# Performance work log

Hardware: AMD Instinct MI355X
Metric: run time of the kernel (lower is better)

The kernel has to match this reference:

```python
import jax, jax.numpy as jnp
import numpy as np

B, N_PER, E_PER = 100, 1000, 12000  # graphs, nodes/graph, edges/graph
N, E = B * N_PER, B * E_PER
K = int(np.ceil(0.8 * N_PER))  # TopKPooling ratio=0.8 -> 800 kept nodes/graph


def setup_inputs() -> dict:
    key = jax.random.key(0)
    ks = jax.random.split(key, 16)
    g = jnp.repeat(jnp.arange(B, dtype=jnp.int64), E_PER)
    src = g * N_PER + jax.random.randint(ks[0], (E,), 0, N_PER)
    dst = g * N_PER + jax.random.randint(ks[1], (E,), 0, N_PER)
    edge_index = jnp.stack([src, dst]).astype(jnp.int64)
    edge_attr = jax.random.uniform(ks[2], (E,), dtype=jnp.float32) + 0.1  # positive edge weights
    x = jax.random.normal(ks[3], (N, 3), dtype=jnp.float32)
    batch = jnp.repeat(jnp.arange(B, dtype=jnp.int64), N_PER)
    s = 0.1
    return {
        'x': x, 'edge_index': edge_index, 'edge_attr': edge_attr, 'batch': batch,
        'conv1_w': jax.random.normal(ks[4], (3, 64), dtype=jnp.float32) * s,
        'conv1_b': jnp.zeros((64,), dtype=jnp.float32),
        'conv2_w': jax.random.normal(ks[5], (64, 64), dtype=jnp.float32) * s,
        'conv2_b': jnp.zeros((64,), dtype=jnp.float32),
        'pool_w': jax.random.normal(ks[6], (64,), dtype=jnp.float32) * s,
        'lin1_w': jax.random.normal(ks[7], (64, 64), dtype=jnp.float32) * s,
        'lin1_b': jnp.zeros((64,), dtype=jnp.float32),
        'lin2_w': jax.random.normal(ks[8], (64, 32), dtype=jnp.float32) * s,
        'lin2_b': jnp.zeros((32,), dtype=jnp.float32),
        'lin3_w': jax.random.normal(ks[9], (32, 1), dtype=jnp.float32) * s,
        'lin3_b': jnp.zeros((1,), dtype=jnp.float32),
    }


def gcn_conv(x, row, col, ew, W, b):
    # PyG GCNConv with edge_weight and implicit self-loops (weight 1):
    # deg[i] = sum_{e: col=i} ew[e] + 1;  norm_e = d^{-1/2}[row]*ew*d^{-1/2}[col]
    h = x @ W  # [N, out]
    deg = jax.ops.segment_sum(ew, col, num_segments=N) + 1.0
    dinv = jax.lax.rsqrt(deg)
    msg = (dinv[row] * ew * dinv[col])[:, None] * h[row]  # [E, out]
    out = jax.ops.segment_sum(msg, col, num_segments=N)
    out = out + (dinv * dinv)[:, None] * h  # self-loop term
    return out + b


def reference(x, edge_index, edge_attr, batch, conv1_w, conv1_b, conv2_w, conv2_b,
              pool_w, lin1_w, lin1_b, lin2_w, lin2_b, lin3_w, lin3_b):
    row, col = edge_index[0], edge_index[1]
    h = jax.nn.relu(gcn_conv(x, row, col, edge_attr, conv1_w, conv1_b))
    x1 = h.reshape(B, N_PER, 64).mean(axis=1)  # global_mean_pool (equal-size graphs)
    h = jax.nn.relu(gcn_conv(h, row, col, edge_attr, conv2_w, conv2_b))
    # TopKPooling: score = tanh(x.w / ||w||), keep top-K per graph, gate by score
    score = jnp.tanh(h @ pool_w / jnp.linalg.norm(pool_w))  # [N]
    score_bn = score.reshape(B, N_PER)
    vals, idx = jax.lax.top_k(score_bn, K)  # [B, K]
    h_bn = h.reshape(B, N_PER, 64)
    h_sel = jnp.take_along_axis(h_bn, idx[..., None], axis=1) * vals[..., None]
    x2 = h_sel.mean(axis=1)  # global_mean_pool on pooled graph
    z = x1 + x2
    z = jax.nn.relu(z @ lin1_w + lin1_b)
    z = jax.nn.relu(z @ lin2_w + lin2_b)  # dropout is identity in eval mode
    out = jax.nn.sigmoid(z @ lin3_w + lin3_b)[:, 0]
    return out
```

## Files before the change

### kernel.cpp

```cpp
#include <hip/hip_runtime.h>

#define B_G   100
#define N_PER 1000
#define E_PER 12000
#define NTOT  (B_G * N_PER)
#define ETOT  (B_G * E_PER)
#define KSEL  800
#define EPT   12

#define CSRB  0u
#define ENDB  4915200u
#define H2B   5324800u
#define KEYB  11878400u
#define X1BB  12697600u
#define WSNEED 12723200u

typedef __attribute__((ext_vector_type(8))) short short8;
typedef __attribute__((ext_vector_type(4))) float float4_;

__device__ __forceinline__ unsigned short f2bf(float f) {
    unsigned u = __float_as_uint(f);
    u += 0x7fffu + ((u >> 16) & 1u);
    return (unsigned short)(u >> 16);
}
__device__ __forceinline__ float upk(unsigned q) {
    return __uint_as_float(q & 0xFFFF0000u);
}
__device__ __forceinline__ float dec_raw(unsigned byte7f) {
    return __uint_as_float(byte7f << 20);
}
__device__ __forceinline__ unsigned enc_fp8(float z) {
    unsigned u = __float_as_uint(z * 0x1p-120f);
    u += 0x7FFFFu + ((u >> 20) & 1u);
    return u >> 20;
}

#define BUILD_BODY(PRE) do {                                                   \
    int esrc[EPT], edst[EPT]; float eww[EPT];                                  \
    int ne = (tid < (E_PER - (EPT - 1) * 1024)) ? EPT : EPT - 1;               \
    _Pragma("unroll")                                                          \
    for (int i = 0; i < EPT; i++) {                                            \
        if (i < ne) {                                                          \
            int e = tid + i * 1024;                                            \
            esrc[i] = ei[ebase + e] - gbase;                                   \
            edst[i] = ei[ETOT + ebase + e] - gbase;                            \
            eww[i]  = ew[ebase + e];                                           \
        }                                                                      \
    }                                                                          \
    ends[tid] = 0;                                                             \
    PRE                                                                        \
    __syncthreads();                                                           \
    _Pragma("unroll")                                                          \
    for (int i = 0; i < EPT; i++)                                              \
        if (i < ne) atomicAdd(&ends[edst[i]], 1);                              \
    __syncthreads();                                                           \
    int v = ends[tid];                                                         \
    int sc = v;                                                                \
    _Pragma("unroll")                                                          \
    for (int m = 1; m < 64; m <<= 1) {                                         \
        int t = __shfl_up(sc, m);                                              \
        if (lane >= m) sc += t;                                                \
    }                                                                          \
    if (lane == 63) wpart[wid] = sc;                                           \
    __syncthreads();                                                           \
    if (tid < 16) {                                                            \
        int s2 = wpart[tid];                                                   \
        _Pragma("unroll")                                                      \
        for (int m = 1; m < 16; m <<= 1) {                                     \
            int t = __shfl_up(s2, m);                                          \
            if (tid >= m) s2 += t;                                             \
        }                                                                      \
        wpart[tid] = s2;                                                       \
    }                                                                          \
    __syncthreads();                                                           \
    int incl = sc + (wid > 0 ? wpart[wid - 1] : 0);                            \
    ends[tid] = incl;                                                          \
    posc[tid] = incl - v;                                                      \
    __syncthreads();                                                           \
    _Pragma("unroll")                                                          \
    for (int i = 0; i < EPT; i++)                                              \
        if (i < ne) {                                                          \
            int p = atomicAdd(&posc[edst[i]], 1);                              \
            csr[p] = ((unsigned)f2bf(eww[i]) << 16) | (unsigned)esrc[i];       \
        }                                                                      \
    __syncthreads();                                                           \
} while (0)

#define REST_BODY() do {                                                       \
    float dmy = 0.f;                                                           \
    int s0i = 0, e0i = 0;                                                      \
    if (tid < N_PER) {                                                         \
        s0i = tid ? ends[tid - 1] : 0;                                         \
        e0i = ends[tid];                                                       \
        float s0 = 0.f, s1 = 0.f;                                              \
        int k = s0i;                                                           \
        for (; k + 2 <= e0i; k += 2) { s0 += upk(csr[k]); s1 += upk(csr[k + 1]); } \
        if (k < e0i) s0 += upk(csr[k]);                                        \
        dmy = rsqrtf(s0 + s1 + 1.0f);                                          \
        dl[tid] = dmy;                                                         \
        xl[tid * 3 + 0] *= dmy;                                                \
        xl[tid * 3 + 1] *= dmy;                                                \
        xl[tid * 3 + 2] *= dmy;                                                \
    }                                                                          \
    __syncthreads();                                                           \
    if (tid < N_PER) {                                                         \
        float a0 = xl[tid * 3 + 0], a1 = xl[tid * 3 + 1], a2 = xl[tid * 3 + 2];\
        for (int k = s0i; k < e0i; k++) {                                      \
            unsigned q = csr[k];                                               \
            int i0 = (int)(q & 0xFFFFu) * 3;                                   \
            float wv = upk(q);                                                 \
            a0 += wv * xl[i0]; a1 += wv * xl[i0 + 1]; a2 += wv * xl[i0 + 2];   \
        }                                                                      \
        aggv[tid * 3 + 0] = dmy * a0;                                          \
        aggv[tid * 3 + 1] = dmy * a1;                                          \
        aggv[tid * 3 + 2] = dmy * a2;                                          \
    }                                                                          \
    __syncthreads();                                                           \
    {                                                                          \
        float w0 = w1[lane], w1v = w1[64 + lane], w2v = w1[128 + lane], bf = b1[lane]; \
        float* sred = (float*)(uA + 12288);                                    \
        float px = 0.f;                                                        \
        int chunk = (lane & 31) >> 3;                                          \
        int word  = ((lane >= 32) ? 2 : 0) + ((lane & 7) >> 2);                \
        for (int node = wid; node < N_PER; node += 16) {                       \
            float a0 = aggv[node * 3], a1 = aggv[node * 3 + 1], a2 = aggv[node * 3 + 2]; \
            float hv = fmaxf(a0 * w0 + a1 * w1v + a2 * w2v + bf, 0.f);         \
            px += hv;                                                          \
            unsigned byte = enc_fp8(dl[node] * hv);                            \
            unsigned t1 = __shfl_xor(byte, 1);                                 \
            unsigned v16 = (lane & 1) ? (t1 | (byte << 8)) : (byte | (t1 << 8)); \
            unsigned t2 = __shfl_xor(v16, 2);                                  \
            unsigned v32 = (lane & 2) ? (t2 | (v16 << 16)) : (v16 | (t2 << 16)); \
            if ((lane & 3) == 0) {                                             \
                int cs = chunk ^ ((node >> 1) & 3);                            \
                *(unsigned*)(zs + node * 64 + cs * 16 + word * 4) = v32;       \
            }                                                                  \
        }                                                                      \
        sred[wid * 64 + lane] = px;                                            \
        __syncthreads();                                                       \
        if (tid < 64) {                                                        \
            float t = 0.f;                                                     \
            for (int r = 0; r < 16; r++) t += sred[r * 64 + tid];              \
            x1b[tid] = t * (1.0f / N_PER);                                     \
        }                                                                      \
    }                                                                          \
} while (0)

#define CONV2_TI(TI, AF0, AF1) do {                                            \
    const int t_ = wid + (TI) * 16;                                            \
    const int li_ = t_ * 16 + nloc;                                            \
    const bool valid_ = li_ < N_PER;                                           \
    float acc_[16];                                                            \
    int s_ = 0, cn_ = 0;                                                       \
    if (valid_) {                                                              \
        uint4 rv_ = *(const uint4*)(zs + li_ * 64 + ((kgrp ^ ((li_ >> 1) & 3)) << 4)); \
        _Pragma("unroll")                                                      \
        for (int j = 0; j < 4; j++) {                                          \
            acc_[j]      = dec_raw((rv_.x >> (8 * j)) & 0x7Fu);                \
            acc_[4 + j]  = dec_raw((rv_.y >> (8 * j)) & 0x7Fu);                \
            acc_[8 + j]  = dec_raw((rv_.z >> (8 * j)) & 0x7Fu);                \
            acc_[12 + j] = dec_raw((rv_.w >> (8 * j)) & 0x7Fu);                \
        }                                                                      \
        s_ = li_ ? ends[li_ - 1] : 0;                                          \
        cn_ = ends[li_] - s_;                                                  \
    } else {                                                                   \
        _Pragma("unroll")                                                      \
        for (int j = 0; j < 16; j++) acc_[j] = 0.f;                            \
    }                                                                          \
    int mx_ = cn_;                                                             \
    _Pragma("unroll")                                                          \
    for (int m = 1; m < 16; m <<= 1) mx_ = max(mx_, __shfl_xor(mx_, m));       \
    for (int k = 0; k < mx_; k++) {                                            \
        if (k < cn_) {                                                         \
            unsigned q_ = csr[s_ + k];                                         \
            int src_ = (int)(q_ & 0xFFFFu);                                    \
            float wv_ = upk(q_);                                               \
            uint4 rv_ = *(const uint4*)(zs + src_ * 64 + ((kgrp ^ ((src_ >> 1) & 3)) << 4)); \
            _Pragma("unroll")                                                  \
            for (int j = 0; j < 4; j++) {                                      \
                acc_[j]      += wv_ * dec_raw((rv_.x >> (8 * j)) & 0x7Fu);     \
                acc_[4 + j]  += wv_ * dec_raw((rv_.y >> (8 * j)) & 0x7Fu);     \
                acc_[8 + j]  += wv_ * dec_raw((rv_.z >> (8 * j)) & 0x7Fu);     \
                acc_[12 + j] += wv_ * dec_raw((rv_.w >> (8 * j)) & 0x7Fu);     \
            }                                                                  \
        }                                                                      \
    }                                                                          \
    float scale_ = (valid_ ? dl[li_] : 0.f) * 0x1p120f;                        \
    _Pragma("unroll")                                                          \
    for (int j = 0; j < 8; j++) {                                              \
        AF0[j] = (short)f2bf(scale_ * acc_[j]);                                \
        AF1[j] = (short)f2bf(scale_ * acc_[8 + j]);                            \
    }                                                                          \
} while (0)

#define W2_TI(TI, AF0, AF1) do {                                               \
    const int t_ = wid + (TI) * 16;                                            \
    if (t_ < 63) {                                                             \
        float4_ accv_[4];                                                      \
        _Pragma("unroll")                                                      \
        for (int c = 0; c < 4; ++c) accv_[c] = (float4_){0.f, 0.f, 0.f, 0.f};  \
        _Pragma("unroll")                                                      \
        for (int c = 0; c < 4; ++c) {                                          \
            accv_[c] = __builtin_amdgcn_mfma_f32_16x16x32_bf16(AF0, Bf[0][c], accv_[c], 0, 0, 0); \
            accv_[c] = __builtin_amdgcn_mfma_f32_16x16x32_bf16(AF1, Bf[1][c], accv_[c], 0, 0, 0); \
        }                                                                      \
        _Pragma("unroll")                                                      \
        for (int r2 = 0; r2 < 4; ++r2) {                                       \
            int li2_ = t_ * 16 + kgrp * 4 + r2;                                \
            bool valid2_ = li2_ < N_PER;                                       \
            float sp_ = 0.f;                                                   \
            _Pragma("unroll")                                                  \
            for (int c = 0; c < 4; ++c) {                                      \
                float hv_ = fmaxf(accv_[c][r2] + b2c[c], 0.f);                 \
                sp_ += hv_ * pwc[c];                                           \
                if (valid2_) zs[li2_ * 64 + c * 16 + nloc] = (unsigned char)enc_fp8(hv_); \
            }                                                                  \
            _Pragma("unroll")                                                  \
            for (int m = 1; m < 16; m <<= 1) sp_ += __shfl_xor(sp_, m);        \
            if (valid2_ && nloc == 0) {                                        \
                float scv_ = tanhf(sp_ * invn);                                \
                unsigned bits_ = __float_as_uint(scv_);                        \
                unsigned u_ = (bits_ & 0x80000000u) ? ~bits_ : (bits_ | 0x80000000u); \
                keys[li2_] = ((unsigned long long)u_ << 32) | (unsigned)(1023 - li2_); \
            }                                                                  \
        }                                                                      \
    }                                                                          \
} while (0)

#define W2_SETUP() do {                                                        \
    _Pragma("unroll")                                                          \
    for (int kh = 0; kh < 2; ++kh)                                             \
        _Pragma("unroll")                                                      \
        for (int c = 0; c < 4; ++c) {                                          \
            short8 t;                                                          \
            _Pragma("unroll")                                                  \
            for (int j = 0; j < 8; ++j)                                        \
                t[j] = (short)f2bf(w2[(kh * 32 + kgrp * 8 + j) * 64 + c * 16 + nloc]); \
            Bf[kh][c] = t;                                                     \
        }                                                                      \
    _Pragma("unroll")                                                          \
    for (int c = 0; c < 4; ++c) {                                              \
        b2c[c] = b2[c * 16 + nloc];                                            \
        pwc[c] = pw[c * 16 + nloc];                                            \
    }                                                                          \
    {                                                                          \
        float p = pw[lane], pn = p * p;                                        \
        _Pragma("unroll")                                                      \
        for (int m = 32; m; m >>= 1) pn += __shfl_xor(pn, m);                  \
        invn = rsqrtf(pn);                                                     \
    }                                                                          \
} while (0)

#define TAIL_BODY(OUTIDX) do {                                                 \
    {                                                                          \
        unsigned long long key = keys[tid];                                    \
        for (int k = 2; k <= 1024; k <<= 1) {                                  \
            for (int j = k >> 1; j > 0; j >>= 1) {                             \
                bool desc = (tid & k) == 0;                                    \
                unsigned long long p;                                          \
                if (j >= 64) {                                                 \
                    keys[tid] = key;                                           \
                    __syncthreads();                                           \
                    p = keys[tid ^ j];                                         \
                    __syncthreads();                                           \
                } else {                                                       \
                    p = __shfl_xor(key, j);                                    \
                }                                                              \
                bool low = (tid & j) == 0;                                     \
                bool sw = low ? (desc ? (key < p) : (key > p))                 \
                              : (desc ? (p < key) : (p > key));                \
                if (sw) key = p;                                               \
            }                                                                  \
        }                                                                      \
        keys[tid] = key;                                                       \
    }                                                                          \
    __syncthreads();                                                           \
    {                                                                          \
        int f = tid & 63, w16 = tid >> 6;                                      \
        float acc2 = 0.f;                                                      \
        for (int r = w16; r < KSEL; r += 16) {                                 \
            unsigned long long key = keys[r];                                  \
            int idx = 1023 - (int)(key & 0xFFFFFFFFu);                         \
            unsigned u = (unsigned)(key >> 32);                                \
            unsigned bits = (u & 0x80000000u) ? (u & 0x7FFFFFFFu) : ~u;        \
            float valS = __uint_as_float(bits) * 0x1p120f;                     \
            acc2 += valS * dec_raw((unsigned)zs[idx * 64 + f] & 0x7Fu);        \
        }                                                                      \
        red[tid] = acc2;                                                       \
    }                                                                          \
    __syncthreads();                                                           \
    if (tid < 64) {                                                            \
        float s2 = 0.f;                                                        \
        for (int ww = 0; ww < 16; ww++) s2 += red[ww * 64 + tid];              \
        zbuf[tid] = x1b[tid] + s2 * (1.0f / KSEL);                             \
    }                                                                          \
    __syncthreads();                                                           \
    if (tid < 64) {                                                            \
        float a = l1b[tid];                                                    \
        for (int k = 0; k < 64; k++) a += zbuf[k] * l1w[k * 64 + tid];         \
        a1buf[tid] = fmaxf(a, 0.f);                                            \
    }                                                                          \
    __syncthreads();                                                           \
    if (tid < 32) {                                                            \
        float a = l2b[tid];                                                    \
        for (int k = 0; k < 64; k++) a += a1buf[k] * l2w[k * 32 + tid];        \
        a2buf[tid] = fmaxf(a, 0.f);                                            \
    }                                                                          \
    __syncthreads();                                                           \
    if (tid == 0) {                                                            \
        float t = l3b[0];                                                      \
        for (int k = 0; k < 32; k++) t += a2buf[k] * l3w[k];                   \
        out[OUTIDX] = 1.0f / (1.0f + expf(-t));                                \
    }                                                                          \
} while (0)

#define SMEM_DECLS()                                                           \
    __shared__ __align__(16) unsigned char smem[136832];                       \
    unsigned char* zs = smem;                                                  \
    float* xl = (float*)smem;                                                  \
    unsigned* csr = (unsigned*)(smem + 64000);                                 \
    int*   ends = (int*)(smem + 112000);                                       \
    float* dl   = (float*)(smem + 116096);                                     \
    int*   posc = (int*)(smem + 116096);                                       \
    int*   wpart = (int*)(smem + 120192);                                      \
    float* x1b   = (float*)(smem + 120192);                                    \
    unsigned char* uA = smem + 120448;                                         \
    float* aggv = (float*)uA;                                                  \
    (void)posc; (void)wpart; (void)aggv;

__global__ __launch_bounds__(1024) void k_build(
    const int* __restrict__ ei, const float* __restrict__ ew,
    unsigned char* __restrict__ ws) {
    __shared__ __align__(16) unsigned csr[12000];
    __shared__ int ends[1024];
    __shared__ int posc[1024];
    __shared__ int wpart[16];
    int g = blockIdx.x, tid = threadIdx.x;
    int wid = tid >> 6, lane = tid & 63;
    int gbase = g * N_PER, ebase = g * E_PER;
    BUILD_BODY();
    {
        uint4* cw = (uint4*)(ws + CSRB + (size_t)g * 49152);
        const uint4* cs = (const uint4*)csr;
        for (int i = tid; i < 3000; i += 1024) cw[i] = cs[i];
        ((int*)(ws + ENDB + (size_t)g * 4096))[tid] = ends[tid];
    }
}

__global__ __launch_bounds__(1024)
__attribute__((amdgpu_waves_per_eu(4, 4))) void k_mid(
    const float* __restrict__ x,
    const float* __restrict__ w1, const float* __restrict__ b1,
    const float* __restrict__ w2, const float* __restrict__ b2,
    const float* __restrict__ pw, unsigned char* __restrict__ ws) {
    SMEM_DECLS();
    int g = blockIdx.x >> 1, half = blockIdx.x & 1, tid = threadIdx.x;
    int wid = tid >> 6, lane = tid & 63;
    int gbase = g * N_PER;
    {
        const uint4* cs = (const uint4*)(ws + CSRB + (size_t)g * 49152);
        uint4* cd = (uint4*)csr;
        for (int i = tid; i < 3000; i += 1024) cd[i] = cs[i];
        ends[tid] = ((const int*)(ws + ENDB + (size_t)g * 4096))[tid];
        for (int i = tid; i < N_PER * 3; i += 1024) xl[i] = x[(size_t)gbase * 3 + i];
    }
    __syncthreads();
    REST_BODY();
    int kgrp = lane >> 4, nloc = lane & 15;
    const int tiA = half * 2, tiB = half * 2 + 1;
    short8 AfAa, AfAb, AfBa, AfBb;
    CONV2_TI(tiA, AfAa, AfAb);
    CONV2_TI(tiB, AfBa, AfBb);
    __syncthreads();
    unsigned long long* keys = (unsigned long long*)uA;
    {
        short8 Bf[2][4]; float b2c[4], pwc[4], invn;
        W2_SETUP();
        if (tid >= N_PER) keys[tid] = 0ull;
        W2_TI(tiA, AfAa, AfAb);
        W2_TI(tiB, AfBa, AfBb);
    }
    __syncthreads();
    {
        uint4* d = (uint4*)(ws + H2B + (size_t)g * 65536 + (size_t)half * 32768);
        const uint4* s = (const uint4*)(zs + half * 32768);
        int n = half ? 1952 : 2048;
        for (int i = tid; i < n; i += 1024) d[i] = s[i];
        unsigned long long* kw =
            (unsigned long long*)(ws + KEYB + (size_t)g * 8192);
        for (int i = tid; i < 512; i += 1024)
            kw[half * 512 + i] = keys[half * 512 + i];
        if (!half && tid < 64)
            ((float*)(ws + X1BB + (size_t)g * 256))[tid] = x1b[tid];
    }
}

__global__ __launch_bounds__(1024) void k_tail(
    const float* __restrict__ l1w, const float* __restrict__ l1b,
    const float* __restrict__ l2w, const float* __restrict__ l2b,
    const float* __restrict__ l3w, const float* __restrict__ l3b,
    float* __restrict__ out, const unsigned char* __restrict__ ws) {
    __shared__ __align__(16) unsigned char sm2[77184];
    unsigned char* zs = sm2;
    unsigned long long* keys = (unsigned long long*)(sm2 + 64000);
    float* red   = (float*)(sm2 + 72192);
    float* x1b   = (float*)(sm2 + 76288);
    float* a1buf = (float*)(sm2 + 76544);
    float* a2buf = (float*)(sm2 + 76800);
    float* zbuf  = (float*)(sm2 + 76928);
    int g = blockIdx.x, tid = threadIdx.x;
    {
        uint4* hd = (uint4*)zs;
        const uint4* hs = (const uint4*)(ws + H2B + (size_t)g * 65536);
        for (int i = tid; i < 4000; i += 1024) hd[i] = hs[i];
        keys[tid] = ((const unsigned long long*)(ws + KEYB + (size_t)g * 8192))[tid];
        if (tid < 64) x1b[tid] = ((const float*)(ws + X1BB + (size_t)g * 256))[tid];
    }
    __syncthreads();
    TAIL_BODY(g);
}

__global__ __launch_bounds__(1024)
__attribute__((amdgpu_waves_per_eu(4, 4))) void k_all_single(
    const int* __restrict__ ei, const float* __restrict__ ew,
    const float* __restrict__ x,
    const float* __restrict__ w1, const float* __restrict__ b1,
    const float* __restrict__ w2, const float* __restrict__ b2,
    const float* __restrict__ pw,
    const float* __restrict__ l1w, const float* __restrict__ l1b,
    const float* __restrict__ l2w, const float* __restrict__ l2b,
    const float* __restrict__ l3w, const float* __restrict__ l3b,
    float* __restrict__ out) {
    SMEM_DECLS();
    int g = blockIdx.x, tid = threadIdx.x;
    int wid = tid >> 6, lane = tid & 63;
    int gbase = g * N_PER, ebase = g * E_PER;
    BUILD_BODY(for (int i = tid; i < N_PER * 3; i += 1024) xl[i] = x[(size_t)gbase * 3 + i];);
    REST_BODY();
    int kgrp = lane >> 4, nloc = lane & 15;
    short8 Af0a, Af0b, Af1a, Af1b, Af2a, Af2b, Af3a, Af3b;
    CONV2_TI(0, Af0a, Af0b);
    CONV2_TI(1, Af1a, Af1b);
    CONV2_TI(2, Af2a, Af2b);
    CONV2_TI(3, Af3a, Af3b);
    __syncthreads();
    unsigned long long* keys = (unsigned long long*)uA;
    {
        short8 Bf[2][4]; float b2c[4], pwc[4], invn;
        W2_SETUP();
        if (tid >= N_PER) keys[tid] = 0ull;
        W2_TI(0, Af0a, Af0b);
        W2_TI(1, Af1a, Af1b);
        W2_TI(2, Af2a, Af2b);
        W2_TI(3, Af3a, Af3b);
    }
    __syncthreads();
    float* red   = (float*)(uA + 8192);
    float* a1buf = (float*)(uA + 12288);
    float* a2buf = (float*)(uA + 12544);
    float* zbuf  = (float*)(uA + 12672);
    TAIL_BODY(g);
}

extern "C" void kernel_launch(void* const* d_in, const int* in_sizes, int n_in,
                              void* d_out, int out_size, void* d_ws, size_t ws_size,
                              hipStream_t stream) {
    const float* x   = (const float*)d_in[0];
    const int*   ei  = (const int*)d_in[1];
    const float* ew  = (const float*)d_in[2];
    const float* c1w = (const float*)d_in[4];
    const float* c1b = (const float*)d_in[5];
    const float* c2w = (const float*)d_in[6];
    const float* c2b = (const float*)d_in[7];
    const float* pw  = (const float*)d_in[8];
    const float* l1w = (const float*)d_in[9];
    const float* l1b = (const float*)d_in[10];
    const float* l2w = (const float*)d_in[11];
    const float* l2b = (const float*)d_in[12];
    const float* l3w = (const float*)d_in[13];
    const float* l3b = (const float*)d_in[14];
    float* out = (float*)d_out;
    (void)in_sizes; (void)n_in; (void)out_size;

    if (d_ws != nullptr && ws_size >= (size_t)WSNEED) {
        unsigned char* ws = (unsigned char*)d_ws;
        k_build<<<B_G, 1024, 0, stream>>>(ei, ew, ws);
        k_mid<<<2 * B_G, 1024, 0, stream>>>(x, c1w, c1b, c2w, c2b, pw, ws);
        k_tail<<<B_G, 1024, 0, stream>>>(l1w, l1b, l2w, l2b, l3w, l3b, out, ws);
    } else {
        k_all_single<<<B_G, 1024, 0, stream>>>(
            ei, ew, x, c1w, c1b, c2w, c2b, pw,
            l1w, l1b, l2w, l2b, l3w, l3b, out);
    }
}
```

Before: 170.7 us.

## Split conv1 front end across two blocks per graph via new kernel

```diff
diff --git a/kernel.cpp b/kernel.cpp
--- a/kernel.cpp
+++ b/kernel.cpp
@@ -8,12 +8,16 @@
 #define KSEL  800
 #define EPT   12
 
-#define CSRB  0u
-#define ENDB  4915200u
-#define H2B   5324800u
-#define KEYB  11878400u
-#define X1BB  12697600u
-#define WSNEED 12723200u
+#define CSRB   0u
+#define ENDB   4915200u
+#define H2B    5324800u
+#define KEYB   11878400u
+#define X1BB   12697600u
+#define P3NEED 12723200u
+#define DLB    12723200u
+#define ZB     13132800u
+#define SREDB  19532800u
+#define P2NEED 19942400u
 
 typedef __attribute__((ext_vector_type(8))) short short8;
 typedef __attribute__((ext_vector_type(4))) float float4_;
@@ -86,64 +90,62 @@
     __syncthreads();                                                           \
 } while (0)
 
-#define REST_BODY() do {                                                       \
-    float dmy = 0.f;                                                           \
-    int s0i = 0, e0i = 0;                                                      \
+#define WSUM_BODY() do {                                                       \
     if (tid < N_PER) {                                                         \
-        s0i = tid ? ends[tid - 1] : 0;                                         \
-        e0i = ends[tid];                                                       \
+        int s0i = tid ? ends[tid - 1] : 0;                                     \
+        int e0i = ends[tid];                                                   \
         float s0 = 0.f, s1 = 0.f;                                              \
         int k = s0i;                                                           \
         for (; k + 2 <= e0i; k += 2) { s0 += upk(csr[k]); s1 += upk(csr[k + 1]); } \
         if (k < e0i) s0 += upk(csr[k]);                                        \
-        dmy = rsqrtf(s0 + s1 + 1.0f);                                          \
+        float dmy = rsqrtf(s0 + s1 + 1.0f);                                    \
         dl[tid] = dmy;                                                         \
         xl[tid * 3 + 0] *= dmy;                                                \
         xl[tid * 3 + 1] *= dmy;                                                \
         xl[tid * 3 + 2] *= dmy;                                                \
-    }                                                                          \
-    __syncthreads();                                                           \
-    if (tid < N_PER) {                                                         \
-        float a0 = xl[tid * 3 + 0], a1 = xl[tid * 3 + 1], a2 = xl[tid * 3 + 2];\
-        for (int k = s0i; k < e0i; k++) {                                      \
-            unsigned q = csr[k];                                               \
-            int i0 = (int)(q & 0xFFFFu) * 3;                                   \
-            float wv = upk(q);                                                 \
-            a0 += wv * xl[i0]; a1 += wv * xl[i0 + 1]; a2 += wv * xl[i0 + 2];   \
-        }                                                                      \
-        aggv[tid * 3 + 0] = dmy * a0;                                          \
-        aggv[tid * 3 + 1] = dmy * a1;                                          \
-        aggv[tid * 3 + 2] = dmy * a2;                                          \
-    }                                                                          \
-    __syncthreads();                                                           \
-    {                                                                          \
-        float w0 = w1[lane], w1v = w1[64 + lane], w2v = w1[128 + lane], bf = b1[lane]; \
-        float* sred = (float*)(uA + 12288);                                    \
-        float px = 0.f;                                                        \
-        int chunk = (lane & 31) >> 3;                                          \
-        int word  = ((lane >= 32) ? 2 : 0) + ((lane & 7) >> 2);                \
-        for (int node = wid; node < N_PER; node += 16) {                       \
-            float a0 = aggv[node * 3], a1 = aggv[node * 3 + 1], a2 = aggv[node * 3 + 2]; \
-            float hv = fmaxf(a0 * w0 + a1 * w1v + a2 * w2v + bf, 0.f);         \
-            px += hv;                                                          \
-            unsigned byte = enc_fp8(dl[node] * hv);                            \
-            unsigned t1 = __shfl_xor(byte, 1);                                 \
-            unsigned v16 = (lane & 1) ? (t1 | (byte << 8)) : (byte | (t1 << 8)); \
-            unsigned t2 = __shfl_xor(v16, 2);                                  \
-            unsigned v32 = (lane & 2) ? (t2 | (v16 << 16)) : (v16 | (t2 << 16)); \
-            if ((lane & 3) == 0) {                                             \
-                int cs = chunk ^ ((node >> 1) & 3);                            \
-                *(unsigned*)(zs + node * 64 + cs * 16 + word * 4) = v32;       \
-            }                                                                  \
-        }                                                                      \
-        sred[wid * 64 + lane] = px;                                            \
-        __syncthreads();                                                       \
-        if (tid < 64) {                                                        \
-            float t = 0.f;                                                     \
-            for (int r = 0; r < 16; r++) t += sred[r * 64 + tid];              \
-            x1b[tid] = t * (1.0f / N_PER);                                     \
-        }                                                                      \
-    }                                                                          \
+        WSUM_EXTRA                                                             \
+    }                                                                          \
+    __syncthreads();                                                           \
+} while (0)
+
+#define CONV1_NODE(NODE) do {                                                  \
+    int node_ = (NODE);                                                        \
+    int s0_ = node_ ? ends[node_ - 1] : 0;                                     \
+    int e0_ = ends[node_];                                                     \
+    float dm_ = dl[node_];                                                     \
+    float a0 = xl[node_ * 3 + 0], a1 = xl[node_ * 3 + 1], a2 = xl[node_ * 3 + 2]; \
+    for (int k = s0_; k < e0_; k++) {                                          \
+        unsigned q = csr[k];                                                   \
+        int i0 = (int)(q & 0xFFFFu) * 3;                                       \
+        float wv = upk(q);                                                     \
+        a0 += wv * xl[i0]; a1 += wv * xl[i0 + 1]; a2 += wv * xl[i0 + 2];       \
+    }                                                                          \
+    aggv[node_ * 3 + 0] = dm_ * a0;                                            \
+    aggv[node_ * 3 + 1] = dm_ * a1;                                            \
+    aggv[node_ * 3 + 2] = dm_ * a2;                                            \
+} while (0)
+
+#define W1_WAVE(OW, PXSTORE) do {                                              \
+    int ow_ = (OW);                                                            \
+    float w0 = w1[lane], w1v = w1[64 + lane], w2v = w1[128 + lane], bf = b1[lane]; \
+    float px = 0.f;                                                            \
+    int chunk = (lane & 31) >> 3;                                              \
+    int word  = ((lane >= 32) ? 2 : 0) + ((lane & 7) >> 2);                    \
+    for (int node = ow_; node < N_PER; node += 16) {                           \
+        float a0 = aggv[node * 3], a1 = aggv[node * 3 + 1], a2 = aggv[node * 3 + 2]; \
+        float hv = fmaxf(a0 * w0 + a1 * w1v + a2 * w2v + bf, 0.f);             \
+        px += hv;                                                              \
+        unsigned byte = enc_fp8(dl[node] * hv);                                \
+        unsigned t1 = __shfl_xor(byte, 1);                                     \
+        unsigned v16 = (lane & 1) ? (t1 | (byte << 8)) : (byte | (t1 << 8));   \
+        unsigned t2 = __shfl_xor(v16, 2);                                      \
+        unsigned v32 = (lane & 2) ? (t2 | (v16 << 16)) : (v16 | (t2 << 16));   \
+        if ((lane & 3) == 0) {                                                 \
+            int cs = chunk ^ ((node >> 1) & 3);                                \
+            *(unsigned*)(zs + node * 64 + cs * 16 + word * 4) = v32;           \
+        }                                                                      \
+    }                                                                          \
+    PXSTORE                                                                    \
 } while (0)
 
 #define CONV2_TI(TI, AF0, AF1) do {                                            \
@@ -193,7 +195,7 @@
     }                                                                          \
 } while (0)
 
-#define W2_TI(TI, AF0, AF1) do {                                               \
+#define W2_TI(TI, AF0, AF1, KEYS) do {                                         \
     const int t_ = wid + (TI) * 16;                                            \
     if (t_ < 63) {                                                             \
         float4_ accv_[4];                                                      \
@@ -221,7 +223,7 @@
                 float scv_ = tanhf(sp_ * invn);                                \
                 unsigned bits_ = __float_as_uint(scv_);                        \
                 unsigned u_ = (bits_ & 0x80000000u) ? ~bits_ : (bits_ | 0x80000000u); \
-                keys[li2_] = ((unsigned long long)u_ << 32) | (unsigned)(1023 - li2_); \
+                (KEYS)[li2_] = ((unsigned long long)u_ << 32) | (unsigned)(1023 - li2_); \
             }                                                                  \
         }                                                                      \
     }                                                                          \
@@ -326,7 +328,7 @@
     float* x1b   = (float*)(smem + 120192);                                    \
     unsigned char* uA = smem + 120448;                                         \
     float* aggv = (float*)uA;                                                  \
-    (void)posc; (void)wpart; (void)aggv;
+    (void)posc; (void)wpart; (void)aggv; (void)x1b; (void)zs;
 
 __global__ __launch_bounds__(1024) void k_build(
     const int* __restrict__ ei, const float* __restrict__ ew,
@@ -347,6 +349,83 @@
     }
 }
 
+#define WSUM_EXTRA if (h == 0) dlws[tid] = dmy;
+__global__ __launch_bounds__(1024)
+__attribute__((amdgpu_waves_per_eu(4, 4))) void k_front2(
+    const float* __restrict__ x,
+    const float* __restrict__ w1, const float* __restrict__ b1,
+    unsigned char* __restrict__ ws) {
+    SMEM_DECLS();
+    int g = blockIdx.x >> 1, h = blockIdx.x & 1, tid = threadIdx.x;
+    int wid = tid >> 6, lane = tid & 63;
+    int gbase = g * N_PER;
+    float* dlws = (float*)(ws + DLB + (size_t)g * 4096);
+    {
+        const uint4* cs = (const uint4*)(ws + CSRB + (size_t)g * 49152);
+        uint4* cd = (uint4*)csr;
+        for (int i = tid; i < 3000; i += 1024) cd[i] = cs[i];
+        ends[tid] = ((const int*)(ws + ENDB + (size_t)g * 4096))[tid];
+        for (int i = tid; i < N_PER * 3; i += 1024) xl[i] = x[(size_t)gbase * 3 + i];
+    }
+    __syncthreads();
+    WSUM_BODY();
+    if (tid < 500) CONV1_NODE(2 * tid + h);
+    __syncthreads();
+    if (wid < 8)
+        W1_WAVE(h + 2 * wid,
+                { ((float*)(ws + SREDB + (size_t)g * 4096))[ow_ * 64 + lane] = px; });
+    __syncthreads();
+    {
+        uint4* zw = (uint4*)(ws + ZB + (size_t)g * 64000);
+        const uint4* zv = (const uint4*)zs;
+        for (int i = tid; i < 4000; i += 1024)
+            if (((i >> 2) & 1) == h) zw[i] = zv[i];
+    }
+}
+#undef WSUM_EXTRA
+
+__global__ __launch_bounds__(1024)
+__attribute__((amdgpu_waves_per_eu(4, 4))) void k_conv2(
+    const float* __restrict__ w2, const float* __restrict__ b2,
+    const float* __restrict__ pw, unsigned char* __restrict__ ws) {
+    SMEM_DECLS();
+    int g = blockIdx.x >> 1, h = blockIdx.x & 1, tid = threadIdx.x;
+    int wid = tid >> 6, lane = tid & 63;
+    unsigned long long* kw = (unsigned long long*)(ws + KEYB + (size_t)g * 8192);
+    {
+        const uint4* zsrc = (const uint4*)(ws + ZB + (size_t)g * 64000);
+        uint4* zd = (uint4*)zs;
+        for (int i = tid; i < 4000; i += 1024) zd[i] = zsrc[i];
+        const uint4* cs = (const uint4*)(ws + CSRB + (size_t)g * 49152);
+        uint4* cd = (uint4*)csr;
+        for (int i = tid; i < 3000; i += 1024) cd[i] = cs[i];
+        ends[tid] = ((const int*)(ws + ENDB + (size_t)g * 4096))[tid];
+        if (tid < N_PER) dl[tid] = ((const float*)(ws + DLB + (size_t)g * 4096))[tid];
+    }
+    __syncthreads();
+    int kgrp = lane >> 4, nloc = lane & 15;
+    const int tiA = h * 2, tiB = h * 2 + 1;
+    short8 AfAa, AfAb, AfBa, AfBb;
+    CONV2_TI(tiA, AfAa, AfAb);
+    CONV2_TI(tiB, AfBa, AfBb);
+    __syncthreads();
+    {
+        short8 Bf[2][4]; float b2c[4], pwc[4], invn;
+        W2_SETUP();
+        if (h == 1 && tid >= N_PER) kw[tid] = 0ull;
+        W2_TI(tiA, AfAa, AfAb, kw);
+        W2_TI(tiB, AfBa, AfBb, kw);
+    }
+    __syncthreads();
+    {
+        uint4* d = (uint4*)(ws + H2B + (size_t)g * 65536);
+        const uint4* s = (const uint4*)zs;
+        int lo = h * 2048, hi = h ? 4000 : 2048;
+        for (int i = lo + tid; i < hi; i += 1024) d[i] = s[i];
+    }
+}
+
+#define WSUM_EXTRA
 __global__ __launch_bounds__(1024)
 __attribute__((amdgpu_waves_per_eu(4, 4))) void k_mid(
     const float* __restrict__ x,
@@ -365,7 +444,19 @@
         for (int i = tid; i < N_PER * 3; i += 1024) xl[i] = x[(size_t)gbase * 3 + i];
     }
     __syncthreads();
-    REST_BODY();
+    WSUM_BODY();
+    if (tid < N_PER) CONV1_NODE(tid);
+    __syncthreads();
+    {
+        float* sred = (float*)(uA + 12288);
+        if (wid < 16) W1_WAVE(wid, { sred[ow_ * 64 + lane] = px; });
+        __syncthreads();
+        if (tid < 64) {
+            float t = 0.f;
+            for (int r = 0; r < 16; r++) t += sred[r * 64 + tid];
+            x1b[tid] = t * (1.0f / N_PER);
+        }
+    }
     int kgrp = lane >> 4, nloc = lane & 15;
     const int tiA = half * 2, tiB = half * 2 + 1;
     short8 AfAa, AfAb, AfBa, AfBb;
@@ -377,8 +468,8 @@
         short8 Bf[2][4]; float b2c[4], pwc[4], invn;
         W2_SETUP();
         if (tid >= N_PER) keys[tid] = 0ull;
-        W2_TI(tiA, AfAa, AfAb);
-        W2_TI(tiB, AfBa, AfBb);
+        W2_TI(tiA, AfAa, AfAb, keys);
+        W2_TI(tiB, AfBa, AfBb, keys);
     }
     __syncthreads();
     {
@@ -386,20 +477,21 @@
         const uint4* s = (const uint4*)(zs + half * 32768);
         int n = half ? 1952 : 2048;
         for (int i = tid; i < n; i += 1024) d[i] = s[i];
-        unsigned long long* kw =
+        unsigned long long* kw2 =
             (unsigned long long*)(ws + KEYB + (size_t)g * 8192);
         for (int i = tid; i < 512; i += 1024)
-            kw[half * 512 + i] = keys[half * 512 + i];
+            kw2[half * 512 + i] = keys[half * 512 + i];
         if (!half && tid < 64)
             ((float*)(ws + X1BB + (size_t)g * 256))[tid] = x1b[tid];
     }
 }
+#undef WSUM_EXTRA
 
 __global__ __launch_bounds__(1024) void k_tail(
     const float* __restrict__ l1w, const float* __restrict__ l1b,
     const float* __restrict__ l2w, const float* __restrict__ l2b,
     const float* __restrict__ l3w, const float* __restrict__ l3b,
-    float* __restrict__ out, const unsigned char* __restrict__ ws) {
+    float* __restrict__ out, const unsigned char* __restrict__ ws, int mode) {
     __shared__ __align__(16) unsigned char sm2[77184];
     unsigned char* zs = sm2;
     unsigned long long* keys = (unsigned long long*)(sm2 + 64000);
@@ -414,12 +506,22 @@
         const uint4* hs = (const uint4*)(ws + H2B + (size_t)g * 65536);
         for (int i = tid; i < 4000; i += 1024) hd[i] = hs[i];
         keys[tid] = ((const unsigned long long*)(ws + KEYB + (size_t)g * 8192))[tid];
-        if (tid < 64) x1b[tid] = ((const float*)(ws + X1BB + (size_t)g * 256))[tid];
+        if (tid < 64) {
+            if (mode) {
+                const float* sr = (const float*)(ws + SREDB + (size_t)g * 4096);
+                float t = 0.f;
+                for (int r = 0; r < 16; r++) t += sr[r * 64 + tid];
+                x1b[tid] = t * (1.0f / N_PER);
+            } else {
+                x1b[tid] = ((const float*)(ws + X1BB + (size_t)g * 256))[tid];
+            }
+        }
     }
     __syncthreads();
     TAIL_BODY(g);
 }
 
+#define WSUM_EXTRA
 __global__ __launch_bounds__(1024)
 __attribute__((amdgpu_waves_per_eu(4, 4))) void k_all_single(
     const int* __restrict__ ei, const float* __restrict__ ew,
@@ -436,7 +538,19 @@
     int wid = tid >> 6, lane = tid & 63;
     int gbase = g * N_PER, ebase = g * E_PER;
     BUILD_BODY(for (int i = tid; i < N_PER * 3; i += 1024) xl[i] = x[(size_t)gbase * 3 + i];);
-    REST_BODY();
+    WSUM_BODY();
+    if (tid < N_PER) CONV1_NODE(tid);
+    __syncthreads();
+    {
+        float* sred = (float*)(uA + 12288);
+        if (wid < 16) W1_WAVE(wid, { sred[ow_ * 64 + lane] = px; });
+        __syncthreads();
+        if (tid < 64) {
+            float t = 0.f;
+            for (int r = 0; r < 16; r++) t += sred[r * 64 + tid];
+            x1b[tid] = t * (1.0f / N_PER);
+        }
+    }
     int kgrp = lane >> 4, nloc = lane & 15;
     short8 Af0a, Af0b, Af1a, Af1b, Af2a, Af2b, Af3a, Af3b;
     CONV2_TI(0, Af0a, Af0b);
@@ -449,10 +563,10 @@
         short8 Bf[2][4]; float b2c[4], pwc[4], invn;
         W2_SETUP();
         if (tid >= N_PER) keys[tid] = 0ull;
-        W2_TI(0, Af0a, Af0b);
-        W2_TI(1, Af1a, Af1b);
-        W2_TI(2, Af2a, Af2b);
-        W2_TI(3, Af3a, Af3b);
+        W2_TI(0, Af0a, Af0b, keys);
+        W2_TI(1, Af1a, Af1b, keys);
+        W2_TI(2, Af2a, Af2b, keys);
+        W2_TI(3, Af3a, Af3b, keys);
     }
     __syncthreads();
     float* red   = (float*)(uA + 8192);
@@ -461,6 +575,7 @@
     float* zbuf  = (float*)(uA + 12672);
     TAIL_BODY(g);
 }
+#undef WSUM_EXTRA
 
 extern "C" void kernel_launch(void* const* d_in, const int* in_sizes, int n_in,
                               void* d_out, int out_size, void* d_ws, size_t ws_size,
@@ -482,11 +597,16 @@
     float* out = (float*)d_out;
     (void)in_sizes; (void)n_in; (void)out_size;
 
-    if (d_ws != nullptr && ws_size >= (size_t)WSNEED) {
-        unsigned char* ws = (unsigned char*)d_ws;
+    unsigned char* ws = (unsigned char*)d_ws;
+    if (d_ws != nullptr && ws_size >= (size_t)P2NEED) {
+        k_build<<<B_G, 1024, 0, stream>>>(ei, ew, ws);
+        k_front2<<<2 * B_G, 1024, 0, stream>>>(x, c1w, c1b, ws);
+        k_conv2<<<2 * B_G, 1024, 0, stream>>>(c2w, c2b, pw, ws);
+        k_tail<<<B_G, 1024, 0, stream>>>(l1w, l1b, l2w, l2b, l3w, l3b, out, ws, 1);
+    } else if (d_ws != nullptr && ws_size >= (size_t)P3NEED) {
         k_build<<<B_G, 1024, 0, stream>>>(ei, ew, ws);
         k_mid<<<2 * B_G, 1024, 0, stream>>>(x, c1w, c1b, c2w, c2b, pw, ws);
-        k_tail<<<B_G, 1024, 0, stream>>>(l1w, l1b, l2w, l2b, l3w, l3b, out, ws);
+        k_tail<<<B_G, 1024, 0, stream>>>(l1w, l1b, l2w, l2b, l3w, l3b, out, ws, 0);
     } else {
         k_all_single<<<B_G, 1024, 0, stream>>>(
             ei, ew, x, c1w, c1b, c2w, c2b, pw,
```

New measurement: 174.9 us. 1.02x slower.
